# Optimization experiments

Hardware: AMD Instinct MI355X
Metric: run time of the kernel (lower is better)

Reference implementation:

```python
import jax, jax.numpy as jnp
import numpy as np


def setup_inputs() -> dict:
    key = jax.random.key(0)
    k1, k2, k3 = jax.random.split(key, 3)
    B, L, d = 4, 9, 256
    n_nodes = (B ** L - 1) // (B - 1)  # complete B-ary tree, level order
    vectors = jax.random.normal(k1, (n_nodes, d), dtype=jnp.float32)
    scale = 1.0 / np.sqrt(d)
    Wl = jax.random.normal(k2, (d, d), dtype=jnp.float32) * scale
    Wr = jax.random.normal(k3, (d, d), dtype=jnp.float32) * scale
    return {"vectors": vectors, "Wl": Wl, "Wr": Wr, "branching": B, "n_levels": L}


def reference(vectors, Wl, Wr, branching, n_levels):
    # Complete branching-ary tree stored in level (BFS) order.
    # Leaf: h = vector. Internal: h = tanh(sum_i lc_i*Wl@h_i + rc_i*Wr@h_i + vector)
    B = int(branching)
    L = int(n_levels)
    sizes = [B ** l for l in range(L)]
    offsets = np.concatenate([[0], np.cumsum(sizes)])
    ind = jnp.arange(1, B + 1, dtype=vectors.dtype)
    if B > 1:
        lc = (B - ind) / (B - 1)   # [B]
        rc = (ind - 1) / (B - 1)
    else:
        lc = jnp.full((B,), 0.5, dtype=vectors.dtype)
        rc = jnp.full((B,), 0.5, dtype=vectors.dtype)
    # leaves
    h = vectors[offsets[L - 1]:offsets[L]]  # [B^(L-1), d]
    for l in range(L - 2, -1, -1):
        n_par = sizes[l]
        hl = (h @ Wl.T).reshape(n_par, B, -1)  # [n_par, B, d]
        hr = (h @ Wr.T).reshape(n_par, B, -1)
        contrib = (lc[None, :, None] * hl + rc[None, :, None] * hr).sum(axis=1)
        h = jnp.tanh(contrib + vectors[offsets[l]:offsets[l + 1]])
    return h  # root state, [1, d]
```

## Files before the change

### kernel.cpp

```cpp
#include <hip/hip_runtime.h>
#include <math.h>


typedef __bf16 bf16x8 __attribute__((ext_vector_type(8)));
typedef __bf16 bf16x4 __attribute__((ext_vector_type(4)));
typedef float f32x4 __attribute__((ext_vector_type(4)));

__device__ __forceinline__ float fast_tanh(float x) {
    float ax = fabsf(x);
    float t = __builtin_amdgcn_exp2f(ax * -2.885390082f);
    float r = (1.0f - t) * __builtin_amdgcn_rcpf(1.0f + t);
    return copysignf(r, x);
}

__device__ __forceinline__ void kbar(unsigned* cnt, int phase, unsigned nb) {
    __syncthreads();
    if (threadIdx.x == 0) {
        __threadfence();
        __hip_atomic_fetch_add(&cnt[phase], 1u, __ATOMIC_ACQ_REL,
                               __HIP_MEMORY_SCOPE_AGENT);
        while (__hip_atomic_load(&cnt[phase], __ATOMIC_ACQUIRE,
                                 __HIP_MEMORY_SCOPE_AGENT) < nb)
            __builtin_amdgcn_s_sleep(1);
        __threadfence();
    }
    __syncthreads();
}

__global__ __launch_bounds__(256) void cbt_wconv(
    const float* __restrict__ Wl, const float* __restrict__ Wr,
    __bf16* __restrict__ Wfrag)
{
    const int t = blockIdx.x * 256 + threadIdx.x;
    const int L = t & 63;
    const int TJ = t >> 6;
    const int T = TJ & 15;
    const int J = TJ >> 4;
    const int n = J * 16 + (L & 15);
    const int k = T * 32 + (L >> 4) * 8;
    const float* src = (k < 256) ? (Wl + (size_t)n * 256 + k)
                                 : (Wr + (size_t)n * 256 + (k - 256));
    const float4 f0 = *reinterpret_cast<const float4*>(src);
    const float4 f1 = *reinterpret_cast<const float4*>(src + 4);
    bf16x8 o;
    o[0] = (__bf16)f0.x; o[1] = (__bf16)f0.y; o[2] = (__bf16)f0.z; o[3] = (__bf16)f0.w;
    o[4] = (__bf16)f1.x; o[5] = (__bf16)f1.y; o[6] = (__bf16)f1.z; o[7] = (__bf16)f1.w;
    *reinterpret_cast<bf16x8*>(Wfrag + (size_t)t * 8) = o;
}

template <typename CT, typename OT>
__device__ __forceinline__ void mfma_body(
    const CT* __restrict__ h,
    const __bf16* __restrict__ Wfrag,
    const float* __restrict__ vec,
    OT* __restrict__ out,
    int mBase, __bf16* Alds)
{
    const int tid = threadIdx.x;
    const int lane = tid & 63;
    const int w = tid >> 6;
    const int wr = w >> 1, wc = w & 1;

    f32x4 acc[8] = {};

    const int sm  = tid >> 3;
    const int skq = (tid & 7) * 4;
    const CT* hb = h + (size_t)(mBase + sm) * 1024 + skq;

    float c0[4], c1[4], c2[4], c3[4];
    auto load_h = [&](int k0) {
        if constexpr (sizeof(CT) == 4) {
            const float4 a = *reinterpret_cast<const float4*>(hb + k0);
            const float4 b = *reinterpret_cast<const float4*>(hb + k0 + 256);
            const float4 c = *reinterpret_cast<const float4*>(hb + k0 + 512);
            const float4 d = *reinterpret_cast<const float4*>(hb + k0 + 768);
            c0[0] = a.x; c0[1] = a.y; c0[2] = a.z; c0[3] = a.w;
            c1[0] = b.x; c1[1] = b.y; c1[2] = b.z; c1[3] = b.w;
            c2[0] = c.x; c2[1] = c.y; c2[2] = c.z; c2[3] = c.w;
            c3[0] = d.x; c3[1] = d.y; c3[2] = d.z; c3[3] = d.w;
        } else {
            const bf16x4 a = *reinterpret_cast<const bf16x4*>(hb + k0);
            const bf16x4 b = *reinterpret_cast<const bf16x4*>(hb + k0 + 256);
            const bf16x4 c = *reinterpret_cast<const bf16x4*>(hb + k0 + 512);
            const bf16x4 d = *reinterpret_cast<const bf16x4*>(hb + k0 + 768);
#pragma unroll
            for (int j = 0; j < 4; ++j) {
                c0[j] = (float)a[j]; c1[j] = (float)b[j];
                c2[j] = (float)c[j]; c3[j] = (float)d[j];
            }
        }
    };

    auto store_A = [&](int buf) {
        constexpr float C23 = 2.0f / 3.0f, C13 = 1.0f / 3.0f;
        bf16x4 glh, gll, grh, grl;
#pragma unroll
        for (int j = 0; j < 4; ++j) {
            const float gl = c0[j] + C23 * c1[j] + C13 * c2[j];
            const float gr = C13 * c1[j] + C23 * c2[j] + c3[j];
            glh[j] = (__bf16)gl;
            gll[j] = (__bf16)(gl - (float)glh[j]);
            grh[j] = (__bf16)gr;
            grl[j] = (__bf16)(gr - (float)grh[j]);
        }
        const int o = buf * 5120 + sm * 40 + skq;
        *reinterpret_cast<bf16x4*>(&Alds[o])        = glh;
        *reinterpret_cast<bf16x4*>(&Alds[o + 1280]) = gll;
        *reinterpret_cast<bf16x4*>(&Alds[o + 2560]) = grh;
        *reinterpret_cast<bf16x4*>(&Alds[o + 3840]) = grl;
    };

    bf16x8 bfr[2][8];
    const __bf16* Wb = Wfrag + ((size_t)wc * 8192 + lane) * 8;
    auto load_B = [&](int s, int buf) {
        const __bf16* p = Wb + (size_t)s * 512;
#pragma unroll
        for (int j = 0; j < 8; ++j)
            bfr[buf][j] = *reinterpret_cast<const bf16x8*>(p + (size_t)j * 8192);
    };

    load_h(0);
    load_B(0, 0);
    load_B(8, 1);
    store_A(0);
    load_h(32);
    __syncthreads();

    const int arow = (wr * 16 + (lane & 15)) * 40 + (lane >> 4) * 8;

    for (int T = 0; T < 8; ++T) {
        const int p = (T & 1) * 5120;
        const int q = ((T + 1) & 1);

        if (T < 7) store_A(q);
        if (T < 6) load_h((T + 2) * 32);

        const bf16x8 afLh = *reinterpret_cast<const bf16x8*>(&Alds[p + arow]);
        const bf16x8 afLl = *reinterpret_cast<const bf16x8*>(&Alds[p + arow + 1280]);
#pragma unroll
        for (int j = 0; j < 8; ++j)
            acc[j] = __builtin_amdgcn_mfma_f32_16x16x32_bf16(
                afLh, bfr[0][j], acc[j], 0, 0, 0);
#pragma unroll
        for (int j = 0; j < 8; ++j)
            acc[j] = __builtin_amdgcn_mfma_f32_16x16x32_bf16(
                afLl, bfr[0][j], acc[j], 0, 0, 0);

        if (T < 7) load_B(T + 1, 0);

        const bf16x8 afRh = *reinterpret_cast<const bf16x8*>(&Alds[p + arow + 2560]);
        const bf16x8 afRl = *reinterpret_cast<const bf16x8*>(&Alds[p + arow + 3840]);
#pragma unroll
        for (int j = 0; j < 8; ++j)
            acc[j] = __builtin_amdgcn_mfma_f32_16x16x32_bf16(
                afRh, bfr[1][j], acc[j], 0, 0, 0);
#pragma unroll
        for (int j = 0; j < 8; ++j)
            acc[j] = __builtin_amdgcn_mfma_f32_16x16x32_bf16(
                afRl, bfr[1][j], acc[j], 0, 0, 0);

        if (T < 7) load_B(T + 9, 1);

        if (T < 7) __syncthreads();
    }

    const int q16 = lane >> 4, n16 = lane & 15;
    const int mrow = mBase + wr * 16 + q16 * 4;
#pragma unroll
    for (int j = 0; j < 8; ++j) {
        const int n = wc * 128 + j * 16 + n16;
#pragma unroll
        for (int r = 0; r < 4; ++r) {
            const size_t idx = (size_t)(mrow + r) * 256 + n;
            out[idx] = (OT)fast_tanh(acc[j][r] + vec[idx]);
        }
    }
}

__global__ __launch_bounds__(256, 2) void cbt_l7(
    const float* __restrict__ vectors, const __bf16* __restrict__ Wfrag,
    __bf16* __restrict__ buf7)
{
    __shared__ __align__(16) __bf16 Alds[8 * 32 * 40];
    mfma_body<float, __bf16>(vectors + (size_t)21845 * 256, Wfrag,
                             vectors + (size_t)5461 * 256, buf7,
                             (int)blockIdx.x * 32, Alds);
}

__global__ __launch_bounds__(256, 2) void cbt_l6(
    const __bf16* __restrict__ h, const __bf16* __restrict__ Wfrag,
    const float* __restrict__ vec, float* __restrict__ out,
    unsigned* __restrict__ bar)
{
    if (blockIdx.x == 0 && threadIdx.x < 8) bar[threadIdx.x] = 0;
    __shared__ __align__(16) __bf16 Alds[8 * 32 * 40];
    mfma_body<__bf16, float>(h, Wfrag, vec, out, (int)blockIdx.x * 32, Alds);
}

__device__ __forceinline__ void valu_level(
    const float* __restrict__ h, const float* __restrict__ Wl,
    const float* __restrict__ Wr, const float* __restrict__ vec,
    float* __restrict__ out, int M, int b, float* G)
{
    const int tid = threadIdx.x;
    constexpr float C23 = 2.0f / 3.0f, C13 = 1.0f / 3.0f;
    constexpr int GS = 516;

    const int nelem = M * 512;
    for (int e = tid; e < nelem; e += 256) {
        const int m = e >> 9, k = e & 511;
        const float* hm = h + (size_t)m * 1024;
        float g;
        if (k < 256)
            g = hm[k] + C23 * hm[256 + k] + C13 * hm[512 + k];
        else {
            const int kk = k - 256;
            g = C13 * hm[256 + kk] + C23 * hm[512 + kk] + hm[768 + kk];
        }
        G[m * GS + k] = g;
    }
    __syncthreads();

    const int g16 = tid >> 4, l16 = tid & 15;
    const int nout = M * 8;
    for (int o = g16; o < nout; o += 16) {
        const int m = o >> 3;
        const int n = b * 8 + (o & 7);
        const float* wlp = Wl + (size_t)n * 256;
        const float* wrp = Wr + (size_t)n * 256;
        float acc = 0.0f;
#pragma unroll
        for (int q = 0; q < 8; ++q) {
            const int k = l16 * 4 + q * 64;
            const float4 gv = *reinterpret_cast<const float4*>(&G[m * GS + k]);
            const float4 wv = (q < 4)
                ? *reinterpret_cast<const float4*>(wlp + k)
                : *reinterpret_cast<const float4*>(wrp + (k - 256));
            acc += gv.x * wv.x + gv.y * wv.y + gv.z * wv.z + gv.w * wv.w;
        }
#pragma unroll
        for (int off = 8; off >= 1; off >>= 1)
            acc += __shfl_xor(acc, off, 64);
        if (l16 == 0) {
            const size_t idx = (size_t)m * 256 + n;
            out[idx] = fast_tanh(acc + vec[idx]);
        }
    }
    __syncthreads();
}

__global__ __launch_bounds__(256) void cbt_rest(
    const float* __restrict__ buf6, const __bf16* __restrict__ Wfrag,
    const float* __restrict__ Wl, const float* __restrict__ Wr,
    const float* __restrict__ vectors,
    float* __restrict__ buf5, float* __restrict__ buf4,
    float* __restrict__ buf3, float* __restrict__ buf2,
    float* __restrict__ buf1, float* __restrict__ outF,
    unsigned* __restrict__ bar)
{
    __shared__ __align__(16) float shG[16 * 516];
    __bf16* Alds = (__bf16*)shG;
    const int b = (int)blockIdx.x;
    const unsigned NB = 32;

    mfma_body<float, float>(buf6, Wfrag, vectors + (size_t)341 * 256, buf5,
                            b * 32, Alds);
    kbar(bar, 0, NB);
    if (b < 8)
        mfma_body<float, float>(buf5, Wfrag, vectors + (size_t)85 * 256, buf4,
                                b * 32, Alds);
    kbar(bar, 1, NB);
    if (b < 2)
        mfma_body<float, float>(buf4, Wfrag, vectors + (size_t)21 * 256, buf3,
                                b * 32, Alds);
    kbar(bar, 2, NB);
    valu_level(buf3, Wl, Wr, vectors + (size_t)5 * 256, buf2, 16, b, shG);
    kbar(bar, 3, NB);
    valu_level(buf2, Wl, Wr, vectors + (size_t)1 * 256, buf1, 4, b, shG);
    kbar(bar, 4, NB);
    valu_level(buf1, Wl, Wr, vectors, outF, 1, b, shG);
}

extern "C" void kernel_launch(void* const* d_in, const int* in_sizes, int n_in,
                              void* d_out, int out_size, void* d_ws, size_t ws_size,
                              hipStream_t stream) {
    const float* vectors = (const float*)d_in[0];
    const float* Wl = (const float*)d_in[1];
    const float* Wr = (const float*)d_in[2];
    float* outF = (float*)d_out;

    char* p = (char*)d_ws;
    __bf16* buf7 = (__bf16*)p;           p += (size_t)16384 * 256 * 2;
    float*  buf6 = (float*)p;            p += (size_t)4096 * 256 * 4;
    float*  buf5 = (float*)p;            p += (size_t)1024 * 256 * 4;
    float*  buf4 = (float*)p;            p += (size_t)256 * 256 * 4;
    float*  buf3 = (float*)p;            p += (size_t)64 * 256 * 4;
    float*  buf2 = (float*)p;            p += (size_t)16 * 256 * 4;
    float*  buf1 = (float*)p;            p += (size_t)4 * 256 * 4;
    __bf16* Wfrag = (__bf16*)p;          p += (size_t)16384 * 8 * 2;
    unsigned* bar = (unsigned*)p;

    hipLaunchKernelGGL(cbt_wconv, dim3(64), dim3(256), 0, stream, Wl, Wr, Wfrag);
    hipLaunchKernelGGL(cbt_l7, dim3(512), dim3(256), 0, stream,
                       vectors, Wfrag, buf7);
    hipLaunchKernelGGL(cbt_l6, dim3(128), dim3(256), 0, stream,
                       buf7, Wfrag, vectors + (size_t)1365 * 256, buf6, bar);
    hipLaunchKernelGGL(cbt_rest, dim3(32), dim3(256), 0, stream,
                       buf6, Wfrag, Wl, Wr, vectors,
                       buf5, buf4, buf3, buf2, buf1, outF, bar);
}
```

Before: 226.6 us.

## Shrink tail kernel to 8 blocks and finish upper levels in one block

```diff
diff --git a/kernel.cpp b/kernel.cpp
--- a/kernel.cpp
+++ b/kernel.cpp
@@ -11,20 +11,6 @@
     float t = __builtin_amdgcn_exp2f(ax * -2.885390082f);
     float r = (1.0f - t) * __builtin_amdgcn_rcpf(1.0f + t);
     return copysignf(r, x);
-}
-
-__device__ __forceinline__ void kbar(unsigned* cnt, int phase, unsigned nb) {
-    __syncthreads();
-    if (threadIdx.x == 0) {
-        __threadfence();
-        __hip_atomic_fetch_add(&cnt[phase], 1u, __ATOMIC_ACQ_REL,
-                               __HIP_MEMORY_SCOPE_AGENT);
-        while (__hip_atomic_load(&cnt[phase], __ATOMIC_ACQUIRE,
-                                 __HIP_MEMORY_SCOPE_AGENT) < nb)
-            __builtin_amdgcn_s_sleep(1);
-        __threadfence();
-    }
-    __syncthreads();
 }
 
 __global__ __launch_bounds__(256) void cbt_wconv(
@@ -54,7 +40,7 @@
     const __bf16* __restrict__ Wfrag,
     const float* __restrict__ vec,
     OT* __restrict__ out,
-    int mBase, __bf16* Alds)
+    int mBase, __bf16* Alds, int mLimit)
 {
     const int tid = threadIdx.x;
     const int lane = tid & 63;
@@ -171,8 +157,10 @@
         const int n = wc * 128 + j * 16 + n16;
 #pragma unroll
         for (int r = 0; r < 4; ++r) {
-            const size_t idx = (size_t)(mrow + r) * 256 + n;
-            out[idx] = (OT)fast_tanh(acc[j][r] + vec[idx]);
+            if (mrow + r < mLimit) {
+                const size_t idx = (size_t)(mrow + r) * 256 + n;
+                out[idx] = (OT)fast_tanh(acc[j][r] + vec[idx]);
+            }
         }
     }
 }
@@ -184,7 +172,7 @@
     __shared__ __align__(16) __bf16 Alds[8 * 32 * 40];
     mfma_body<float, __bf16>(vectors + (size_t)21845 * 256, Wfrag,
                              vectors + (size_t)5461 * 256, buf7,
-                             (int)blockIdx.x * 32, Alds);
+                             (int)blockIdx.x * 32, Alds, 1 << 30);
 }
 
 __global__ __launch_bounds__(256, 2) void cbt_l6(
@@ -194,13 +182,14 @@
 {
     if (blockIdx.x == 0 && threadIdx.x < 8) bar[threadIdx.x] = 0;
     __shared__ __align__(16) __bf16 Alds[8 * 32 * 40];
-    mfma_body<__bf16, float>(h, Wfrag, vec, out, (int)blockIdx.x * 32, Alds);
-}
-
-__device__ __forceinline__ void valu_level(
+    mfma_body<__bf16, float>(h, Wfrag, vec, out, (int)blockIdx.x * 32, Alds,
+                             1 << 30);
+}
+
+__device__ __forceinline__ void valu_full(
     const float* __restrict__ h, const float* __restrict__ Wl,
     const float* __restrict__ Wr, const float* __restrict__ vec,
-    float* __restrict__ out, int M, int b, float* G)
+    float* __restrict__ out, int M, float* G)
 {
     const int tid = threadIdx.x;
     constexpr float C23 = 2.0f / 3.0f, C13 = 1.0f / 3.0f;
@@ -222,10 +211,10 @@
     __syncthreads();
 
     const int g16 = tid >> 4, l16 = tid & 15;
-    const int nout = M * 8;
+    const int nout = M * 256;
     for (int o = g16; o < nout; o += 16) {
-        const int m = o >> 3;
-        const int n = b * 8 + (o & 7);
+        const int m = o >> 8;
+        const int n = o & 255;
         const float* wlp = Wl + (size_t)n * 256;
         const float* wrp = Wr + (size_t)n * 256;
         float acc = 0.0f;
@@ -249,7 +238,7 @@
     __syncthreads();
 }
 
-__global__ __launch_bounds__(256) void cbt_rest(
+__global__ __launch_bounds__(256) void cbt_tail(
     const float* __restrict__ buf6, const __bf16* __restrict__ Wfrag,
     const float* __restrict__ Wl, const float* __restrict__ Wr,
     const float* __restrict__ vectors,
@@ -258,27 +247,46 @@
     float* __restrict__ buf1, float* __restrict__ outF,
     unsigned* __restrict__ bar)
 {
-    __shared__ __align__(16) float shG[16 * 516];
-    __bf16* Alds = (__bf16*)shG;
+    __shared__ __align__(16) __bf16 Alds[8 * 32 * 40];
+    float* shG = (float*)Alds;
     const int b = (int)blockIdx.x;
-    const unsigned NB = 32;
-
-    mfma_body<float, float>(buf6, Wfrag, vectors + (size_t)341 * 256, buf5,
-                            b * 32, Alds);
-    kbar(bar, 0, NB);
-    if (b < 8)
-        mfma_body<float, float>(buf5, Wfrag, vectors + (size_t)85 * 256, buf4,
-                                b * 32, Alds);
-    kbar(bar, 1, NB);
-    if (b < 2)
-        mfma_body<float, float>(buf4, Wfrag, vectors + (size_t)21 * 256, buf3,
-                                b * 32, Alds);
-    kbar(bar, 2, NB);
-    valu_level(buf3, Wl, Wr, vectors + (size_t)5 * 256, buf2, 16, b, shG);
-    kbar(bar, 3, NB);
-    valu_level(buf2, Wl, Wr, vectors + (size_t)1 * 256, buf1, 4, b, shG);
-    kbar(bar, 4, NB);
-    valu_level(buf1, Wl, Wr, vectors, outF, 1, b, shG);
+    const int tid = threadIdx.x;
+
+#pragma unroll 1
+    for (int t = 0; t < 4; ++t) {
+        mfma_body<float, float>(buf6, Wfrag, vectors + (size_t)341 * 256, buf5,
+                                (4 * b + t) * 32, Alds, 1 << 30);
+        __syncthreads();
+    }
+    mfma_body<float, float>(buf5, Wfrag, vectors + (size_t)85 * 256, buf4,
+                            b * 32, Alds, 1 << 30);
+    __syncthreads();
+
+    if (tid == 0) {
+        __threadfence();
+        __hip_atomic_fetch_add(&bar[0], 1u, __ATOMIC_ACQ_REL,
+                               __HIP_MEMORY_SCOPE_AGENT);
+    }
+    if (b != 0) return;
+    if (tid == 0) {
+        while (__hip_atomic_load(&bar[0], __ATOMIC_RELAXED,
+                                 __HIP_MEMORY_SCOPE_AGENT) < 8u)
+            __builtin_amdgcn_s_sleep(1);
+        __threadfence();
+    }
+    __syncthreads();
+
+    mfma_body<float, float>(buf4, Wfrag, vectors + (size_t)21 * 256, buf3,
+                            0, Alds, 64);
+    __syncthreads();
+    mfma_body<float, float>(buf4, Wfrag, vectors + (size_t)21 * 256, buf3,
+                            32, Alds, 64);
+    __syncthreads();
+    mfma_body<float, float>(buf3, Wfrag, vectors + (size_t)5 * 256, buf2,
+                            0, Alds, 16);
+    __syncthreads();
+    valu_full(buf2, Wl, Wr, vectors + (size_t)1 * 256, buf1, 4, shG);
+    valu_full(buf1, Wl, Wr, vectors, outF, 1, shG);
 }
 
 extern "C" void kernel_launch(void* const* d_in, const int* in_sizes, int n_in,
@@ -305,7 +313,7 @@
                        vectors, Wfrag, buf7);
     hipLaunchKernelGGL(cbt_l6, dim3(128), dim3(256), 0, stream,
                        buf7, Wfrag, vectors + (size_t)1365 * 256, buf6, bar);
-    hipLaunchKernelGGL(cbt_rest, dim3(32), dim3(256), 0, stream,
+    hipLaunchKernelGGL(cbt_tail, dim3(8), dim3(256), 0, stream,
                        buf6, Wfrag, Wl, Wr, vectors,
                        buf5, buf4, buf3, buf2, buf1, outF, bar);
 }
```

Measured after the change: 483.9 us. 114% more time.
